# Optimization experiments

Measured on AMD Instinct MI355X. Metric: run time of the kernel, lower is better.

## Reference

```python
import math
import jax, jax.numpy as jnp
import numpy as np

SHAPES = [(80, 80), (40, 40), (20, 20), (10, 10)]
BS, LQ, D, NH, NL, NP = 8, 1000, 256, 8, 4, 4
C = D // NH


def _offset_bias():
    # replicates _reset_parameters grid_init bias for sampling_offsets
    thetas = np.arange(NH, dtype=np.float32) * (2.0 * math.pi / NH)
    grid = np.stack([np.cos(thetas), np.sin(thetas)], -1)  # [NH,2]
    grid = grid / np.abs(grid).max(-1, keepdims=True)
    grid = np.tile(grid[:, None, None, :], (1, NL, NP, 1))  # [NH,NL,NP,2]
    for i in range(NP):
        grid[:, :, i, :] *= i + 1
    return jnp.asarray(grid.reshape(-1))


def setup_inputs() -> dict:
    key = jax.random.key(0)
    ks = jax.random.split(key, 8)
    len_v = sum(h * w for h, w in SHAPES)
    s = 1.0 / math.sqrt(D)
    starts = np.cumsum([0] + [h * w for h, w in SHAPES])[:-1]
    return {
        "query": jax.random.normal(ks[0], (BS, LQ, D), jnp.float32),
        "reference_points": jax.random.uniform(ks[1], (BS, LQ, NL, 2), jnp.float32),
        "value": jax.random.normal(ks[2], (BS, len_v, D), jnp.float32),
        "w_off": jax.random.normal(ks[3], (D, NH * NL * NP * 2), jnp.float32) * 0.01,
        "b_off": _offset_bias(),
        "w_attn": jax.random.normal(ks[4], (D, NH * NL * NP), jnp.float32) * 0.01,
        "b_attn": jnp.zeros((NH * NL * NP,), jnp.float32),
        "w_v": jax.random.normal(ks[5], (D, D), jnp.float32) * s,
        "b_v": jnp.zeros((D,), jnp.float32),
        "w_o": jax.random.normal(ks[6], (D, D), jnp.float32) * s,
        "b_o": jnp.zeros((D,), jnp.float32),
        "value_spatial_shapes": jnp.array(SHAPES, jnp.int32),
        "value_level_start_index": jnp.array(starts, jnp.int32),
    }


def _sample(img, grid, H, W):
    # bilinear grid_sample, padding_mode='zeros', align_corners=False
    # img: [B, C, H*W], grid: [B, Q, P, 2] in [-1, 1] -> out [B, C, Q, P]
    x = (grid[..., 0] + 1.0) * (W * 0.5) - 0.5
    y = (grid[..., 1] + 1.0) * (H * 0.5) - 0.5
    x0 = jnp.floor(x)
    y0 = jnp.floor(y)
    fx = x - x0
    fy = y - y0
    x0i = x0.astype(jnp.int32)
    y0i = y0.astype(jnp.int32)

    def gather(xi, yi, w):
        valid = (xi >= 0) & (xi < W) & (yi >= 0) & (yi < H)
        idx = jnp.clip(yi, 0, H - 1) * W + jnp.clip(xi, 0, W - 1)
        B, Q, P = idx.shape
        g = jax.vmap(lambda im, ix: im[:, ix])(img, idx.reshape(B, Q * P))  # [B,C,QP]
        return g.reshape(B, -1, Q, P) * (w * valid)[:, None]

    return (gather(x0i, y0i, (1 - fx) * (1 - fy))
            + gather(x0i + 1, y0i, fx * (1 - fy))
            + gather(x0i, y0i + 1, (1 - fx) * fy)
            + gather(x0i + 1, y0i + 1, fx * fy))


def _forward(query, reference_points, value, w_off, b_off, w_attn, b_attn,
             w_v, b_v, w_o, b_o, shapes):
    bs, lq, _ = query.shape
    v = (value @ w_v + b_v).reshape(bs, -1, NH, C)  # [bs, len_v, NH, C]
    off = (query @ w_off + b_off).reshape(bs, lq, NH, NL, NP, 2)
    attn = jax.nn.softmax((query @ w_attn + b_attn).reshape(bs, lq, NH, NL * NP), axis=-1)
    attn = attn.reshape(bs, lq, NH, NL, NP)
    # offset normalizer is spatial_shapes flipped -> (W, H) per level
    norm = jnp.array([[w, h] for h, w in shapes], dtype=query.dtype)  # [NL,2]
    loc = reference_points[:, :, None, :, None, :] + off / norm[None, None, None, :, None, :]
    grids = 2.0 * loc - 1.0  # [bs,lq,NH,NL,NP,2]
    start = 0
    sampled = []
    for lvl, (H, W) in enumerate(shapes):
        v_l = v[:, start:start + H * W].transpose(0, 2, 3, 1).reshape(bs * NH, C, H * W)
        g_l = grids[:, :, :, lvl].transpose(0, 2, 1, 3, 4).reshape(bs * NH, lq, NP, 2)
        sampled.append(_sample(v_l, g_l, H, W))  # [bs*NH, C, lq, NP]
        start += H * W
    samp = jnp.stack(sampled, axis=3).reshape(bs * NH, C, lq, NL * NP)
    aw = attn.transpose(0, 2, 1, 3, 4).reshape(bs * NH, 1, lq, NL * NP)
    out = (samp * aw).sum(-1).reshape(bs, NH * C, lq).transpose(0, 2, 1)  # [bs,lq,D]
    return out @ w_o + b_o


def reference(query, reference_points, value, w_off, b_off, w_attn, b_attn,
              w_v, b_v, w_o, b_o, value_spatial_shapes, value_level_start_index):
    shapes = [tuple(int(x) for x in r) for r in np.asarray(value_spatial_shapes)]
    return _forward(query, reference_points, value, w_off, b_off, w_attn, b_attn,
                    w_v, b_v, w_o, b_o, shapes)
```

## Files before the change

kernel.cpp:

```cpp
#include <hip/hip_runtime.h>
#include <hip/hip_bf16.h>
#include <math.h>

#define BS     8
#define LQ     1000
#define DMODEL 256
#define NH     8
#define NLV    4
#define NPT    4
#define LEN_V  8500
#define NQ     (BS*LQ)
#define MV     (BS*LEN_V)
#define KS     8

typedef __attribute__((ext_vector_type(8))) short short8;
typedef __attribute__((ext_vector_type(4))) float floatx4;

static __device__ __forceinline__ unsigned short f2bf(float f) {
    __hip_bfloat16 h = __float2bfloat16(f);
    return __builtin_bit_cast(unsigned short, h);
}
static __device__ __forceinline__ float asf(unsigned int u) {
    return __builtin_bit_cast(float, u);
}

static __device__ __forceinline__ void gemm_tile(
    const float* __restrict__ Aptr, const unsigned short* __restrict__ Bfrag,
    const float* __restrict__ bias1, const float* __restrict__ bias2, int nsplit,
    void* __restrict__ Cptr, int M, int N, int bn, int bm,
    bool outbf, unsigned short* As )
{
    const int tid = threadIdx.x;
    const int l   = tid & 63;
    const int w   = tid >> 6;
    const int lm  = l & 15;
    const int lk  = l >> 4;
    const int x7  = lm & 7;

    auto aoff = [&](int j) -> size_t {
        const int slot = j * 256 + tid;
        const int row  = slot >> 5;
        const int gc   = (slot & 31) ^ (row & 7);
        int grow = bm * 64 + row; grow = grow < M ? grow : M - 1;
        return (size_t)grow * 256 + gc * 8;
    };

    float4 ra[8][2];
    #pragma unroll
    for (int j = 0; j < 8; ++j) {
        const float* s = Aptr + aoff(j);
        ra[j][0] = *(const float4*)s;
        ra[j][1] = *(const float4*)(s + 4);
    }

    short8 Bf[2][KS];
    const int u0 = bn * 8 + w * 2;
    #pragma unroll
    for (int j = 0; j < 2; ++j)
        #pragma unroll
        for (int s = 0; s < KS; ++s)
            Bf[j][s] = *(const short8*)(Bfrag + ((size_t)((u0 + j) * KS + s) * 64 + l) * 8);

    #pragma unroll
    for (int j = 0; j < 8; ++j) {
        short8 o;
        o[0] = (short)f2bf(ra[j][0].x); o[1] = (short)f2bf(ra[j][0].y);
        o[2] = (short)f2bf(ra[j][0].z); o[3] = (short)f2bf(ra[j][0].w);
        o[4] = (short)f2bf(ra[j][1].x); o[5] = (short)f2bf(ra[j][1].y);
        o[6] = (short)f2bf(ra[j][1].z); o[7] = (short)f2bf(ra[j][1].w);
        *(short8*)&As[(j * 256 + tid) * 8] = o;
    }
    __syncthreads();

    floatx4 acc[4][2];
    #pragma unroll
    for (int i = 0; i < 4; ++i)
        #pragma unroll
        for (int j = 0; j < 2; ++j)
            #pragma unroll
            for (int r = 0; r < 4; ++r) acc[i][j][r] = 0.f;

    #pragma unroll
    for (int s = 0; s < KS; ++s) {
        short8 afr[4];
        #pragma unroll
        for (int i = 0; i < 4; ++i)
            afr[i] = *(const short8*)(
                &As[(i * 16 + lm) * 256 + (((s * 4 + lk) ^ x7)) * 8]);
        #pragma unroll
        for (int i = 0; i < 4; ++i)
            #pragma unroll
            for (int j = 0; j < 2; ++j)
                acc[i][j] = __builtin_amdgcn_mfma_f32_16x16x32_bf16(
                                afr[i], Bf[j][s], acc[i][j], 0, 0, 0);
    }

    #pragma unroll
    for (int j = 0; j < 2; ++j) {
        const int col = bn * 128 + w * 32 + j * 16 + lm;
        const float bv = (bias2 != nullptr && col >= nsplit) ? bias2[col - nsplit]
                                                             : bias1[col];
        #pragma unroll
        for (int i = 0; i < 4; ++i) {
            const int rbase = bm * 64 + i * 16 + lk * 4;
            #pragma unroll
            for (int r = 0; r < 4; ++r) {
                const int row = rbase + r;
                if (row < M) {
                    const float v = acc[i][j][r] + bv;
                    if (outbf)
                        ((unsigned short*)Cptr)[(size_t)row * N + col] = f2bf(v);
                    else
                        ((float*)Cptr)[(size_t)row * N + col] = v;
                }
            }
        }
    }
}

__global__ __launch_bounds__(256, 3) void gemm_fused(
    const float* __restrict__ value, const float* __restrict__ query,
    const unsigned short* __restrict__ wv_f, const unsigned short* __restrict__ woa_f,
    const float* __restrict__ b_v, const float* __restrict__ b_off,
    const float* __restrict__ b_attn,
    unsigned short* __restrict__ v_proj, float* __restrict__ offattn)
{
    __shared__ unsigned short As[16384];
    int bx = blockIdx.x;
    if (bx < 2128) {
        const int xcd  = bx & 7;
        const int k    = bx >> 3;
        const int tile = xcd * 133 + (k >> 1);
        const int half = k & 1;
        if (tile < 1063)
            gemm_tile(value, wv_f, b_v, nullptr, 1 << 30,
                      v_proj, MV, 256, half, tile, true, As);
    } else {
        bx -= 2128;
        gemm_tile(query, woa_f, b_off, b_attn, 256,
                  offattn, NQ, 384, bx % 3, bx / 3, false, As);
    }
}

__global__ __launch_bounds__(256) void prep_w(
    const float* __restrict__ w_v, const float* __restrict__ w_off,
    const float* __restrict__ w_attn, const float* __restrict__ w_o,
    unsigned short* __restrict__ wv_f, unsigned short* __restrict__ woa_f,
    unsigned short* __restrict__ wo_f)
{
    const int gid = blockIdx.x * 256 + threadIdx.x;
    int chunk, mode;
    if (gid < 8192)               { chunk = gid;         mode = 0; }
    else if (gid < 8192 + 12288)  { chunk = gid - 8192;  mode = 1; }
    else                          { chunk = gid - 20480; mode = 2; }
    const int l = chunk & 63, s = (chunk >> 6) & 7, u = chunk >> 9;
    short8 o;
    #pragma unroll
    for (int j = 0; j < 8; ++j) {
        const int k = s * 32 + (l >> 4) * 8 + j;
        const int n = u * 16 + (l & 15);
        float v;
        if (mode == 0)      v = w_v[k * 256 + n];
        else if (mode == 1) v = (n < 256) ? w_off[k * 256 + n] : w_attn[k * 128 + (n - 256)];
        else                v = w_o[k * 256 + n];
        o[j] = (short)f2bf(v);
    }
    unsigned short* dp = (mode == 0 ? wv_f : mode == 1 ? woa_f : wo_f)
                         + ((size_t)(u * 8 + s) * 64 + l) * 8;
    *(short8*)dp = o;
}

__global__ __launch_bounds__(512) void ms_sample_out(
    const unsigned short* __restrict__ v,
    const float* __restrict__ offattn,
    const float* __restrict__ refp,
    const unsigned short* __restrict__ wo_f,
    const float* __restrict__ b_o,
    float* __restrict__ out)
{
    __shared__ float offx_s[8][16][8];
    __shared__ float offy_s[8][16][8];
    __shared__ float atw_s [8][16][8];
    __shared__ float ref_s [8][8];
    __shared__ unsigned short pA[16][256];

    const int tid  = threadIdx.x;
    const int bswz = blockIdx.x & 7;
    const int iq0  = bswz * 1000 + (blockIdx.x >> 3) * 8;

    {
        const int row = 8 + (tid >> 6);
        const int c4  = (tid & 63) * 4;
        ushort4 z; z.x = 0; z.y = 0; z.z = 0; z.w = 0;
        *(ushort4*)&pA[row][c4] = z;
    }

    if (tid < 64) {
        const int q = tid >> 3, h = tid & 7;
        const float* rowp = offattn + (size_t)(iq0 + q) * 384;
        float lg[16];
        float m = -1e30f;
        #pragma unroll
        for (int i = 0; i < 16; ++i) { lg[i] = rowp[256 + h * 16 + i]; m = fmaxf(m, lg[i]); }
        float s = 0.f;
        #pragma unroll
        for (int i = 0; i < 16; ++i) { lg[i] = __expf(lg[i] - m); s += lg[i]; }
        const float inv = 1.f / s;
        #pragma unroll
        for (int i = 0; i < 16; ++i) atw_s[q][i][h] = lg[i] * inv;
        #pragma unroll
        for (int i = 0; i < 16; ++i) {
            offx_s[q][i][h] = rowp[(h * 16 + i) * 2 + 0];
            offy_s[q][i][h] = rowp[(h * 16 + i) * 2 + 1];
        }
        if (h == 0) {
            #pragma unroll
            for (int i = 0; i < 8; ++i) ref_s[q][i] = refp[(size_t)(iq0 + q) * 8 + i];
        }
    }
    __syncthreads();

    const int q8 = tid >> 6;
    const int cs = tid & 63;
    const int h  = cs >> 3;
    const int s4 = cs & 7;

    float acc[4] = {0.f, 0.f, 0.f, 0.f};
    const unsigned short* vb = v + (size_t)bswz * LEN_V * 256 + h * 32 + s4 * 4;
    const int Hs[4] = {80, 40, 20, 10};
    const int st[4] = {0, 6400, 8000, 8400};

    #pragma unroll
    for (int lvl = 0; lvl < NLV; ++lvl) {
        const int W = Hs[lvl];
        const float bx = ref_s[q8][lvl * 2 + 0] * (float)W - 0.5f;
        const float by = ref_s[q8][lvl * 2 + 1] * (float)W - 0.5f;
        const unsigned short* vl = vb + (size_t)st[lvl] * 256;
        #pragma unroll
        for (int p = 0; p < NPT; ++p) {
            const int lp = lvl * 4 + p;
            const float x  = bx + offx_s[q8][lp][h];
            const float y  = by + offy_s[q8][lp][h];
            const float at = atw_s[q8][lp][h];
            const float x0f = floorf(x), y0f = floorf(y);
            const float fx = x - x0f, fy = y - y0f;
            const int x0 = (int)x0f, y0 = (int)y0f;
            const int x1 = x0 + 1,   y1 = y0 + 1;
            const int cx0 = min(max(x0, 0), W - 1);
            const int cx1 = min(max(x1, 0), W - 1);
            const int cy0 = min(max(y0, 0), W - 1);
            const int cy1 = min(max(y1, 0), W - 1);
            const float vx0 = (x0 >= 0 && x0 < W) ? 1.f : 0.f;
            const float vx1 = (x1 >= 0 && x1 < W) ? 1.f : 0.f;
            const float vy0 = (y0 >= 0 && y0 < W) ? 1.f : 0.f;
            const float vy1 = (y1 >= 0 && y1 < W) ? 1.f : 0.f;
            const float w00 = at * (1.f - fx) * (1.f - fy) * vx0 * vy0;
            const float w01 = at * fx * (1.f - fy) * vx1 * vy0;
            const float w10 = at * (1.f - fx) * fy * vx0 * vy1;
            const float w11 = at * fx * fy * vx1 * vy1;
            const unsigned short* r0 = vl + (size_t)(cy0 * W) * 256;
            const unsigned short* r1 = vl + (size_t)(cy1 * W) * 256;
            const uint2 d00 = *(const uint2*)(r0 + (size_t)cx0 * 256);
            const uint2 d01 = *(const uint2*)(r0 + (size_t)cx1 * 256);
            const uint2 d10 = *(const uint2*)(r1 + (size_t)cx0 * 256);
            const uint2 d11 = *(const uint2*)(r1 + (size_t)cx1 * 256);
            acc[0] += w00 * asf(d00.x << 16) + w01 * asf(d01.x << 16)
                    + w10 * asf(d10.x << 16) + w11 * asf(d11.x << 16);
            acc[1] += w00 * asf(d00.x & 0xffff0000u) + w01 * asf(d01.x & 0xffff0000u)
                    + w10 * asf(d10.x & 0xffff0000u) + w11 * asf(d11.x & 0xffff0000u);
            acc[2] += w00 * asf(d00.y << 16) + w01 * asf(d01.y << 16)
                    + w10 * asf(d10.y << 16) + w11 * asf(d11.y << 16);
            acc[3] += w00 * asf(d00.y & 0xffff0000u) + w01 * asf(d01.y & 0xffff0000u)
                    + w10 * asf(d10.y & 0xffff0000u) + w11 * asf(d11.y & 0xffff0000u);
        }
    }

    {
        ushort4 o;
        o.x = f2bf(acc[0]); o.y = f2bf(acc[1]);
        o.z = f2bf(acc[2]); o.w = f2bf(acc[3]);
        *(ushort4*)&pA[q8][cs * 4] = o;
    }
    __syncthreads();

    const int l  = tid & 63;
    const int w8 = tid >> 6;
    const int lm = l & 15;
    const int lk = l >> 4;

    floatx4 oacc[2];
    #pragma unroll
    for (int j = 0; j < 2; ++j)
        #pragma unroll
        for (int r = 0; r < 4; ++r) oacc[j][r] = 0.f;

    #pragma unroll
    for (int s = 0; s < KS; ++s) {
        const short8 a = *(const short8*)&pA[lm][(s * 4 + lk) * 8];
        #pragma unroll
        for (int j = 0; j < 2; ++j) {
            const short8 b = *(const short8*)(
                wo_f + ((size_t)((w8 * 2 + j) * KS + s) * 64 + l) * 8);
            oacc[j] = __builtin_amdgcn_mfma_f32_16x16x32_bf16(a, b, oacc[j], 0, 0, 0);
        }
    }

    if (lk < 2) {
        #pragma unroll
        for (int j = 0; j < 2; ++j) {
            const int col = w8 * 32 + j * 16 + lm;
            const float bo = b_o[col];
            #pragma unroll
            for (int r = 0; r < 4; ++r) {
                const int q = lk * 4 + r;
                out[(size_t)(iq0 + q) * 256 + col] = oacc[j][r] + bo;
            }
        }
    }
}

extern "C" void kernel_launch(void* const* d_in, const int* in_sizes, int n_in,
                              void* d_out, int out_size, void* d_ws, size_t ws_size,
                              hipStream_t stream)
{
    const float* query  = (const float*)d_in[0];
    const float* refp   = (const float*)d_in[1];
    const float* value  = (const float*)d_in[2];
    const float* w_off  = (const float*)d_in[3];
    const float* b_off  = (const float*)d_in[4];
    const float* w_attn = (const float*)d_in[5];
    const float* b_attn = (const float*)d_in[6];
    const float* w_v    = (const float*)d_in[7];
    const float* b_v    = (const float*)d_in[8];
    const float* w_o    = (const float*)d_in[9];
    const float* b_o    = (const float*)d_in[10];
    (void)d_in[11]; (void)d_in[12];

    float* out = (float*)d_out;

    char* ws = (char*)d_ws;
    unsigned short* v_proj  = (unsigned short*)ws;
    float*          offattn = (float*)(ws + 34816000);
    unsigned short* wv_f    = (unsigned short*)(ws + 47104000);
    unsigned short* woa_f   = (unsigned short*)(ws + 47235072);
    unsigned short* wo_f    = (unsigned short*)(ws + 47431680);

    dim3 blk(256);

    hipLaunchKernelGGL(prep_w, dim3(112), blk, 0, stream,
                       w_v, w_off, w_attn, w_o, wv_f, woa_f, wo_f);
    hipLaunchKernelGGL(gemm_fused, dim3(2503), blk, 0, stream,
                       value, query, wv_f, woa_f, b_v, b_off, b_attn, v_proj, offattn);
    hipLaunchKernelGGL(ms_sample_out, dim3(1000), dim3(512), 0, stream,
                       v_proj, offattn, refp, wo_f, b_o, out);
}
```

Baseline: 181.7 us.

## Process multiple M-tiles per GEMM block with register double-buffered A prefetch

Each GEMM block now iterates over up to three consecutive 64-row tiles, loading the B fragments once and prefetching the next A tile into a second register buffer while converting and computing the current one. The grid shrinks accordingly and the previous XCD-aware tile remapping is removed. This aims to amortize B loads and hide global load latency behind MFMA work, at the cost of higher register pressure and fewer blocks for load balancing.

```diff
diff --git a/kernel.cpp b/kernel.cpp
--- a/kernel.cpp
+++ b/kernel.cpp
@@ -24,43 +24,24 @@
     return __builtin_bit_cast(float, u);
 }
 
-static __device__ __forceinline__ void gemm_tile(
-    const float* __restrict__ Aptr, const unsigned short* __restrict__ Bfrag,
-    const float* __restrict__ bias1, const float* __restrict__ bias2, int nsplit,
-    void* __restrict__ Cptr, int M, int N, int bn, int bm,
-    bool outbf, unsigned short* As )
-{
-    const int tid = threadIdx.x;
-    const int l   = tid & 63;
-    const int w   = tid >> 6;
-    const int lm  = l & 15;
-    const int lk  = l >> 4;
-    const int x7  = lm & 7;
-
-    auto aoff = [&](int j) -> size_t {
+static __device__ __forceinline__ void issue_tileA(
+    const float* __restrict__ A, int bm, int M, int tid, float4 (&ra)[8][2])
+{
+    #pragma unroll
+    for (int j = 0; j < 8; ++j) {
         const int slot = j * 256 + tid;
         const int row  = slot >> 5;
         const int gc   = (slot & 31) ^ (row & 7);
         int grow = bm * 64 + row; grow = grow < M ? grow : M - 1;
-        return (size_t)grow * 256 + gc * 8;
-    };
-
-    float4 ra[8][2];
-    #pragma unroll
-    for (int j = 0; j < 8; ++j) {
-        const float* s = Aptr + aoff(j);
+        const float* s = A + (size_t)grow * 256 + gc * 8;
         ra[j][0] = *(const float4*)s;
         ra[j][1] = *(const float4*)(s + 4);
     }
-
-    short8 Bf[2][KS];
-    const int u0 = bn * 8 + w * 2;
-    #pragma unroll
-    for (int j = 0; j < 2; ++j)
-        #pragma unroll
-        for (int s = 0; s < KS; ++s)
-            Bf[j][s] = *(const short8*)(Bfrag + ((size_t)((u0 + j) * KS + s) * 64 + l) * 8);
-
+}
+
+static __device__ __forceinline__ void cvt_write(
+    const float4 (&ra)[8][2], unsigned short* As, int tid)
+{
     #pragma unroll
     for (int j = 0; j < 8; ++j) {
         short8 o;
@@ -70,51 +51,99 @@
         o[6] = (short)f2bf(ra[j][1].z); o[7] = (short)f2bf(ra[j][1].w);
         *(short8*)&As[(j * 256 + tid) * 8] = o;
     }
-    __syncthreads();
-
-    floatx4 acc[4][2];
-    #pragma unroll
-    for (int i = 0; i < 4; ++i)
-        #pragma unroll
-        for (int j = 0; j < 2; ++j)
-            #pragma unroll
-            for (int r = 0; r < 4; ++r) acc[i][j][r] = 0.f;
-
-    #pragma unroll
-    for (int s = 0; s < KS; ++s) {
-        short8 afr[4];
-        #pragma unroll
-        for (int i = 0; i < 4; ++i)
-            afr[i] = *(const short8*)(
-                &As[(i * 16 + lm) * 256 + (((s * 4 + lk) ^ x7)) * 8]);
-        #pragma unroll
-        for (int i = 0; i < 4; ++i)
+}
+
+static __device__ __forceinline__ void lds_barrier()
+{
+    asm volatile("s_waitcnt lgkmcnt(0)" ::: "memory");
+    __builtin_amdgcn_s_barrier();
+    __builtin_amdgcn_sched_barrier(0);
+}
+
+static __device__ __forceinline__ void gemm_group(
+    const float* __restrict__ Aptr, const unsigned short* __restrict__ Bfrag,
+    const float* __restrict__ bias1, const float* __restrict__ bias2, int nsplit,
+    void* __restrict__ Cptr, int M, int N, int bn, int g0, int nt,
+    bool outbf, unsigned short* As )
+{
+    const int tid = threadIdx.x;
+    const int l   = tid & 63;
+    const int w   = tid >> 6;
+    const int lm  = l & 15;
+    const int lk  = l >> 4;
+    const int x7  = lm & 7;
+
+    float4 raA[8][2], raB[8][2];
+    issue_tileA(Aptr, g0, M, tid, raA);
+
+    short8 Bf[2][KS];
+    const int u0 = bn * 8 + w * 2;
+    #pragma unroll
+    for (int j = 0; j < 2; ++j)
+        #pragma unroll
+        for (int s = 0; s < KS; ++s)
+            Bf[j][s] = *(const short8*)(Bfrag + ((size_t)((u0 + j) * KS + s) * 64 + l) * 8);
+
+    bool useA = true;
+    for (int i = 0; i < nt; ++i) {
+        const int bm = g0 + i;
+
+        if (useA) {
+            if (i + 1 < nt) issue_tileA(Aptr, bm + 1, M, tid, raB);
+            cvt_write(raA, As, tid);
+        } else {
+            if (i + 1 < nt) issue_tileA(Aptr, bm + 1, M, tid, raA);
+            cvt_write(raB, As, tid);
+        }
+        useA = !useA;
+        lds_barrier();
+
+        floatx4 acc[4][2];
+        #pragma unroll
+        for (int ii = 0; ii < 4; ++ii)
             #pragma unroll
             for (int j = 0; j < 2; ++j)
-                acc[i][j] = __builtin_amdgcn_mfma_f32_16x16x32_bf16(
-                                afr[i], Bf[j][s], acc[i][j], 0, 0, 0);
-    }
-
-    #pragma unroll
-    for (int j = 0; j < 2; ++j) {
-        const int col = bn * 128 + w * 32 + j * 16 + lm;
-        const float bv = (bias2 != nullptr && col >= nsplit) ? bias2[col - nsplit]
-                                                             : bias1[col];
-        #pragma unroll
-        for (int i = 0; i < 4; ++i) {
-            const int rbase = bm * 64 + i * 16 + lk * 4;
-            #pragma unroll
-            for (int r = 0; r < 4; ++r) {
-                const int row = rbase + r;
-                if (row < M) {
-                    const float v = acc[i][j][r] + bv;
-                    if (outbf)
-                        ((unsigned short*)Cptr)[(size_t)row * N + col] = f2bf(v);
-                    else
-                        ((float*)Cptr)[(size_t)row * N + col] = v;
+                #pragma unroll
+                for (int r = 0; r < 4; ++r) acc[ii][j][r] = 0.f;
+
+        #pragma unroll
+        for (int s = 0; s < KS; ++s) {
+            short8 afr[4];
+            #pragma unroll
+            for (int ii = 0; ii < 4; ++ii)
+                afr[ii] = *(const short8*)(
+                    &As[(ii * 16 + lm) * 256 + (((s * 4 + lk) ^ x7)) * 8]);
+            #pragma unroll
+            for (int ii = 0; ii < 4; ++ii)
+                #pragma unroll
+                for (int j = 0; j < 2; ++j)
+                    acc[ii][j] = __builtin_amdgcn_mfma_f32_16x16x32_bf16(
+                                    afr[ii], Bf[j][s], acc[ii][j], 0, 0, 0);
+        }
+
+        #pragma unroll
+        for (int j = 0; j < 2; ++j) {
+            const int col = bn * 128 + w * 32 + j * 16 + lm;
+            const float bv = (bias2 != nullptr && col >= nsplit) ? bias2[col - nsplit]
+                                                                 : bias1[col];
+            #pragma unroll
+            for (int ii = 0; ii < 4; ++ii) {
+                const int rbase = bm * 64 + ii * 16 + lk * 4;
+                #pragma unroll
+                for (int r = 0; r < 4; ++r) {
+                    const int row = rbase + r;
+                    if (row < M) {
+                        const float v = acc[ii][j][r] + bv;
+                        if (outbf)
+                            ((unsigned short*)Cptr)[(size_t)row * N + col] = f2bf(v);
+                        else
+                            ((float*)Cptr)[(size_t)row * N + col] = v;
+                    }
                 }
             }
         }
+
+        lds_barrier();
     }
 }
 
@@ -126,19 +155,20 @@
     unsigned short* __restrict__ v_proj, float* __restrict__ offattn)
 {
     __shared__ unsigned short As[16384];
-    int bx = blockIdx.x;
-    if (bx < 2128) {
-        const int xcd  = bx & 7;
-        const int k    = bx >> 3;
-        const int tile = xcd * 133 + (k >> 1);
-        const int half = k & 1;
-        if (tile < 1063)
-            gemm_tile(value, wv_f, b_v, nullptr, 1 << 30,
-                      v_proj, MV, 256, half, tile, true, As);
+    const int bx = blockIdx.x;
+    if (bx < 710) {
+        const int grp = bx >> 1, half = bx & 1;
+        const int g0 = grp * 3;
+        const int nt = min(3, 1063 - g0);
+        gemm_group(value, wv_f, b_v, nullptr, 1 << 30,
+                   v_proj, MV, 256, half, g0, nt, true, As);
     } else {
-        bx -= 2128;
-        gemm_tile(query, woa_f, b_off, b_attn, 256,
-                  offattn, NQ, 384, bx % 3, bx / 3, false, As);
+        const int ob = bx - 710;
+        const int third = ob % 3, grp = ob / 3;
+        const int g0 = grp * 3;
+        const int nt = min(3, 125 - g0);
+        gemm_group(query, woa_f, b_off, b_attn, 256,
+                   offattn, NQ, 384, third, g0, nt, false, As);
     }
 }
 
@@ -349,7 +379,7 @@
 
     hipLaunchKernelGGL(prep_w, dim3(112), blk, 0, stream,
                        w_v, w_off, w_attn, w_o, wv_f, woa_f, wo_f);
-    hipLaunchKernelGGL(gemm_fused, dim3(2503), blk, 0, stream,
+    hipLaunchKernelGGL(gemm_fused, dim3(836), blk, 0, stream,
                        value, query, wv_f, woa_f, b_v, b_off, b_attn, v_proj, offattn);
     hipLaunchKernelGGL(ms_sample_out, dim3(1000), dim3(512), 0, stream,
                        v_proj, offattn, refp, wo_f, b_o, out);
```

Measured after the change: 341.3 us. +87.9%, slower.

## Pipeline value projection with double-buffered LDS DMA and register-resident weights

Applied to the files above, without the earlier changes.

Replaces the per-tile value-projection GEMM with a persistent-style routine. Each block keeps the full weight fragments in registers and streams eight 32-row tiles of the fp32 value input into LDS through direct global-to-LDS loads, double-buffered so the next tile loads while the current one runs on MFMA. This removes repeated weight loads and hides global load latency. In exchange, LDS grows to 64KB, launch bounds drop to 2 blocks per CU, the grid shrinks to 641 blocks, and the XCD-aware tile mapping is dropped.

```diff
diff --git a/kernel.cpp b/kernel.cpp
--- a/kernel.cpp
+++ b/kernel.cpp
@@ -24,6 +24,105 @@
     return __builtin_bit_cast(float, u);
 }
 
+static __device__ __forceinline__ void dma16(const void* g, void* lds) {
+    __builtin_amdgcn_global_load_lds(
+        (const __attribute__((address_space(1))) unsigned int*)g,
+        (__attribute__((address_space(3))) unsigned int*)lds,
+        16, 0, 0);
+}
+
+static __device__ __forceinline__ void vproj_pipe(
+    const float* __restrict__ A, const unsigned short* __restrict__ Bfrag,
+    const float* __restrict__ bias, unsigned short* __restrict__ C,
+    int t0, int nt, float* __restrict__ Asf )
+{
+    const int tid = threadIdx.x;
+    const int l   = tid & 63;
+    const int w   = tid >> 6;
+    const int lm  = l & 15;
+    const int lk  = l >> 4;
+
+    short8 Bf[4][KS];
+    #pragma unroll
+    for (int j = 0; j < 4; ++j)
+        #pragma unroll
+        for (int s = 0; s < KS; ++s)
+            Bf[j][s] = *(const short8*)(Bfrag + ((size_t)((w * 4 + j) * KS + s) * 64 + l) * 8);
+
+    auto dma_tile = [&](int t, int buf) {
+        float* dst = Asf + buf * 8192;
+        #pragma unroll
+        for (int j = 0; j < 8; ++j) {
+            const int slot = j * 256 + tid;
+            const int row  = slot >> 6;
+            const int gsrc = (slot & 63) ^ (row & 15);
+            dma16(A + (size_t)(t * 32 + row) * 256 + gsrc * 4,
+                  dst + (size_t)(j * 256 + w * 64) * 4);
+        }
+    };
+
+    dma_tile(t0, 0);
+    int buf = 0;
+    for (int i = 0; i < nt; ++i) {
+        if (i + 1 < nt) {
+            dma_tile(t0 + i + 1, buf ^ 1);
+            asm volatile("s_waitcnt vmcnt(8)" ::: "memory");
+        } else {
+            asm volatile("s_waitcnt vmcnt(0)" ::: "memory");
+        }
+        __builtin_amdgcn_s_barrier();
+        __builtin_amdgcn_sched_barrier(0);
+
+        const float* As_f = Asf + buf * 8192;
+        floatx4 acc[2][4];
+        #pragma unroll
+        for (int ii = 0; ii < 2; ++ii)
+            #pragma unroll
+            for (int j = 0; j < 4; ++j)
+                #pragma unroll
+                for (int r = 0; r < 4; ++r) acc[ii][j][r] = 0.f;
+
+        #pragma unroll
+        for (int s = 0; s < KS; ++s) {
+            short8 afr[2];
+            #pragma unroll
+            for (int ii = 0; ii < 2; ++ii) {
+                const int row = ii * 16 + lm;
+                const int cb  = s * 8 + lk * 2;
+                const float4 a0 = *(const float4*)&As_f[row * 256 + ((cb    ) ^ lm) * 4];
+                const float4 a1 = *(const float4*)&As_f[row * 256 + ((cb + 1) ^ lm) * 4];
+                afr[ii][0] = (short)f2bf(a0.x); afr[ii][1] = (short)f2bf(a0.y);
+                afr[ii][2] = (short)f2bf(a0.z); afr[ii][3] = (short)f2bf(a0.w);
+                afr[ii][4] = (short)f2bf(a1.x); afr[ii][5] = (short)f2bf(a1.y);
+                afr[ii][6] = (short)f2bf(a1.z); afr[ii][7] = (short)f2bf(a1.w);
+            }
+            #pragma unroll
+            for (int ii = 0; ii < 2; ++ii)
+                #pragma unroll
+                for (int j = 0; j < 4; ++j)
+                    acc[ii][j] = __builtin_amdgcn_mfma_f32_16x16x32_bf16(
+                                    afr[ii], Bf[j][s], acc[ii][j], 0, 0, 0);
+        }
+
+        #pragma unroll
+        for (int j = 0; j < 4; ++j) {
+            const int col = w * 64 + j * 16 + lm;
+            const float bv = bias[col];
+            #pragma unroll
+            for (int ii = 0; ii < 2; ++ii) {
+                const int rbase = (t0 + i) * 32 + ii * 16 + lk * 4;
+                #pragma unroll
+                for (int r = 0; r < 4; ++r)
+                    C[(size_t)(rbase + r) * 256 + col] = f2bf(acc[ii][j][r] + bv);
+            }
+        }
+
+        __builtin_amdgcn_s_barrier();
+        __builtin_amdgcn_sched_barrier(0);
+        buf ^= 1;
+    }
+}
+
 static __device__ __forceinline__ void gemm_tile(
     const float* __restrict__ Aptr, const unsigned short* __restrict__ Bfrag,
     const float* __restrict__ bias1, const float* __restrict__ bias2, int nsplit,
@@ -118,27 +217,23 @@
     }
 }
 
-__global__ __launch_bounds__(256, 3) void gemm_fused(
+__global__ __launch_bounds__(256, 2) void gemm_fused(
     const float* __restrict__ value, const float* __restrict__ query,
     const unsigned short* __restrict__ wv_f, const unsigned short* __restrict__ woa_f,
     const float* __restrict__ b_v, const float* __restrict__ b_off,
     const float* __restrict__ b_attn,
     unsigned short* __restrict__ v_proj, float* __restrict__ offattn)
 {
-    __shared__ unsigned short As[16384];
-    int bx = blockIdx.x;
-    if (bx < 2128) {
-        const int xcd  = bx & 7;
-        const int k    = bx >> 3;
-        const int tile = xcd * 133 + (k >> 1);
-        const int half = k & 1;
-        if (tile < 1063)
-            gemm_tile(value, wv_f, b_v, nullptr, 1 << 30,
-                      v_proj, MV, 256, half, tile, true, As);
+    __shared__ __align__(16) char sh[65536];
+    const int bx = blockIdx.x;
+    if (bx < 266) {
+        const int t0 = bx * 8;
+        const int nt = min(8, 2125 - t0);
+        vproj_pipe(value, wv_f, b_v, v_proj, t0, nt, (float*)sh);
     } else {
-        bx -= 2128;
+        const int ob = bx - 266;
         gemm_tile(query, woa_f, b_off, b_attn, 256,
-                  offattn, NQ, 384, bx % 3, bx / 3, false, As);
+                  offattn, NQ, 384, ob % 3, ob / 3, false, (unsigned short*)sh);
     }
 }
 
@@ -349,7 +444,7 @@
 
     hipLaunchKernelGGL(prep_w, dim3(112), blk, 0, stream,
                        w_v, w_off, w_attn, w_o, wv_f, woa_f, wo_f);
-    hipLaunchKernelGGL(gemm_fused, dim3(2503), blk, 0, stream,
+    hipLaunchKernelGGL(gemm_fused, dim3(641), blk, 0, stream,
                        value, query, wv_f, woa_f, b_v, b_off, b_attn, v_proj, offattn);
     hipLaunchKernelGGL(ms_sample_out, dim3(1000), dim3(512), 0, stream,
                        v_proj, offattn, refp, wo_f, b_o, out);
```

Result: faster. 174.0 us (-4.2%).
